# Performance work log

Measured on AMD Instinct MI355X. Metric: run time of the kernel, lower is better.

## Reference

```python
import jax, jax.numpy as jnp
import numpy as np

B, LQ, LK, QD, KD, VD, H = 8, 128, 1024, 128, 128, 128, 128
NEG_INF = -1e6  # d2l masked_softmax fill value


def setup_inputs() -> dict:
    key = jax.random.key(0)
    k1, k2, k3, k4, k5, k6, k7 = jax.random.split(key, 7)
    return {
        "queries": jax.random.normal(k1, (B, LQ, QD), dtype=jnp.float32),
        "keys": jax.random.normal(k2, (B, LK, KD), dtype=jnp.float32),
        "values": jax.random.normal(k3, (B, LK, VD), dtype=jnp.float32),
        "valid_lens": jax.random.randint(k4, (B,), 0, LK),
        # learned params: torch Linear(in,out,bias=False); stored here as [in,out]
        "W_q": jax.random.normal(k5, (QD, H), dtype=jnp.float32) / np.sqrt(QD),
        "W_k": jax.random.normal(k6, (KD, H), dtype=jnp.float32) / np.sqrt(KD),
        "w_v": jax.random.normal(k7, (H,), dtype=jnp.float32) / np.sqrt(H),
    }


def reference(queries, keys, values, valid_lens, W_q, W_k, w_v):
    q = jnp.einsum("blq,qh->blh", queries, W_q)            # [B,Lq,H]
    k = jnp.einsum("bsk,kh->bsh", keys, W_k)               # [B,Lk,H]
    features = jnp.tanh(q[:, :, None, :] + k[:, None, :, :])  # [B,Lq,Lk,H]
    scores = jnp.einsum("blsh,h->bls", features, w_v)      # [B,Lq,Lk]
    mask = jnp.arange(LK)[None, None, :] < valid_lens[:, None, None]
    scores = jnp.where(mask, scores, NEG_INF)
    attn = jax.nn.softmax(scores, axis=-1)                 # dropout p=0.0 -> identity
    return jnp.einsum("bls,bsv->blv", attn, values)        # [B,Lq,Vd]
```

## Files before the change

### kernel.cpp

```cpp
#include <hip/hip_runtime.h>
#include <hip/hip_fp16.h>

#define B_   8
#define LQ_  128
#define LK_  1024
#define H_   128

__device__ float        g_eq  [B_ * LQ_ * H_];
__device__ uint4        g_ekT4[B_ * (H_ / 4) * (LK_ / 2)];
__device__ unsigned int g_vh  [B_ * LK_ * (H_ / 2)];

#define C2LOG2E 2.8853900817779268f

__global__ __launch_bounds__(256) void proj_conv(const float* __restrict__ q,
                                                 const float* __restrict__ k,
                                                 const float* __restrict__ Wq,
                                                 const float* __restrict__ Wk,
                                                 const float* __restrict__ values) {
    const int bx = blockIdx.x, ch = blockIdx.y;
    const int t = threadIdx.x;
    if (bx >= 288) {
        const int idx = ((bx - 288) + (ch << 9)) * 256 + t;
        float4 v = *(const float4*)(values + (size_t)idx * 4);
        __half2 p0 = __floats2half2_rn(v.x, v.y);
        __half2 p1 = __floats2half2_rn(v.z, v.w);
        *(uint2*)(g_vh + (size_t)idx * 2) =
            make_uint2(*(unsigned int*)&p0, *(unsigned int*)&p1);
        return;
    }
    __shared__ float Ws[H_ * 64];
    __shared__ float Xs[32 * H_];
    const bool isq = (bx < 32);
    const float* X; const float* W; int r0;
    if (isq) { X = q; W = Wq; r0 = bx * 32; }
    else     { X = k; W = Wk; r0 = (bx - 32) * 32; }

    #pragma unroll
    for (int u = 0; u < 8; ++u) {
        int p = u * 256 + t;
        int kk = p >> 4, c4 = p & 15;
        *(float4*)(Ws + kk * 64 + c4 * 4) = *(const float4*)(W + kk * H_ + ch * 64 + c4 * 4);
    }
    #pragma unroll
    for (int u = 0; u < 4; ++u) {
        int idx = u * 256 + t;
        int r = idx >> 5, c = idx & 31;
        *(float4*)(Xs + r * H_ + c * 4) = *(const float4*)(X + (size_t)(r0 + r) * H_ + c * 4);
    }
    __syncthreads();

    const int rr = t >> 4;
    const int cc = t & 15;
    float acc[2][4] = {};
    #pragma unroll 4
    for (int kk = 0; kk < H_; ++kk) {
        float4 w4 = *(const float4*)(Ws + kk * 64 + cc * 4);
        float x0 = Xs[(rr * 2) * H_ + kk];
        float x1 = Xs[(rr * 2 + 1) * H_ + kk];
        acc[0][0] = fmaf(x0, w4.x, acc[0][0]); acc[0][1] = fmaf(x0, w4.y, acc[0][1]);
        acc[0][2] = fmaf(x0, w4.z, acc[0][2]); acc[0][3] = fmaf(x0, w4.w, acc[0][3]);
        acc[1][0] = fmaf(x1, w4.x, acc[1][0]); acc[1][1] = fmaf(x1, w4.y, acc[1][1]);
        acc[1][2] = fmaf(x1, w4.z, acc[1][2]); acc[1][3] = fmaf(x1, w4.w, acc[1][3]);
    }
    if (isq) {
        #pragma unroll
        for (int i = 0; i < 2; ++i) {
            float4 o;
            o.x = __builtin_amdgcn_exp2f(acc[i][0] * C2LOG2E);
            o.y = __builtin_amdgcn_exp2f(acc[i][1] * C2LOG2E);
            o.z = __builtin_amdgcn_exp2f(acc[i][2] * C2LOG2E);
            o.w = __builtin_amdgcn_exp2f(acc[i][3] * C2LOG2E);
            *(float4*)(g_eq + (size_t)(r0 + rr * 2 + i) * H_ + ch * 64 + cc * 4) = o;
        }
    } else {
        const int b  = r0 >> 10;
        const int s0 = (r0 & 1023) + rr * 2;
        const int h4 = ch * 16 + cc;
        uint4 pk;
        #pragma unroll
        for (int j = 0; j < 4; ++j) {
            float e0 = __builtin_amdgcn_exp2f(acc[0][j] * C2LOG2E);
            float e1 = __builtin_amdgcn_exp2f(acc[1][j] * C2LOG2E);
            __half2 p = __floats2half2_rn(e0, e1);
            ((unsigned int*)&pk)[j] = *(unsigned int*)&p;
        }
        g_ekT4[((size_t)b * (H_ / 4) + h4) * (LK_ / 2) + (s0 >> 1)] = pk;
    }
}

__global__ __launch_bounds__(512, 8) void fused_attn(const int* __restrict__ valid_lens,
                                                     const float* __restrict__ w_v,
                                                     float* __restrict__ out) {
    __shared__ float sc[LK_];
    __shared__ float sred[8];
    __shared__ float rinv_s;
    __shared__ float part[16][H_];
    const int t = threadIdx.x;
    const int lane = t & 63, wid = t >> 6;
    const int b = blockIdx.x >> 7, l = blockIdx.x & 127;
    int valid = valid_lens[b];
    valid = min(max(valid, 0), LK_);

    const int s0 = 2 * t;
    float e0 = 0.0f, e1 = 0.0f;
    if (valid == 0) {
        for (int i = t; i < LK_; i += 512) sc[i] = 1.0f;
    } else if (s0 < valid) {
        const float* __restrict__ q0 = g_eq + (size_t)(b * LQ_ + l) * H_;
        const uint4* __restrict__ ek = g_ekT4 + (size_t)b * (H_ / 4) * (LK_ / 2) + t;
        float a0 = 0.0f, a1 = 0.0f;
        #pragma unroll
        for (int hb = 0; hb < 4; ++hb) {
            uint4 r[8];
            #pragma unroll
            for (int i = 0; i < 8; ++i)
                r[i] = ek[(size_t)(hb * 8 + i) * (LK_ / 2)];
            #pragma unroll
            for (int i = 0; i < 8; ++i) {
                #pragma unroll
                for (int j = 0; j < 4; ++j) {
                    unsigned int uj = ((const unsigned int*)&r[i])[j];
                    float2 ef = __half22float2(*(const __half2*)&uj);
                    const int h = (hb * 8 + i) * 4 + j;
                    const float qh = q0[h], wh = w_v[h];
                    a0 = fmaf(wh, __builtin_amdgcn_rcpf(fmaf(qh, ef.x, 1.0f)), a0);
                    a1 = fmaf(wh, __builtin_amdgcn_rcpf(fmaf(qh, ef.y, 1.0f)), a1);
                }
            }
        }
        e0 = __builtin_amdgcn_exp2f(a0 * (-2.0f * 1.44269504f));
        float e1f = __builtin_amdgcn_exp2f(a1 * (-2.0f * 1.44269504f));
        *(float2*)(sc + s0) = make_float2(e0, e1f);
        e1 = (s0 + 1 < valid) ? e1f : 0.0f;
    }
    float ps = e0 + e1;
    #pragma unroll
    for (int kk = 32; kk; kk >>= 1) ps += __shfl_xor(ps, kk, 64);
    if (lane == 0) sred[wid] = ps;
    __syncthreads();
    if (t == 0) {
        float s8 = ((sred[0] + sred[1]) + (sred[2] + sred[3]))
                 + ((sred[4] + sred[5]) + (sred[6] + sred[7]));
        rinv_s = (valid == 0) ? (1.0f / 1024.0f) : (1.0f / s8);
    }
    __syncthreads();
    const float rinv = rinv_s;
    const int n = (valid == 0) ? LK_ : valid;

    const int c = t >> 5;
    const int v4 = t & 31;
    const uint2* vb = (const uint2*)g_vh + (size_t)b * LK_ * (H_ / 4) + v4;
    float ax = 0.0f, ay = 0.0f, az = 0.0f, aw = 0.0f;
    int s = c;
    for (; s + 16 * 7 < n; s += 16 * 8) {
        uint2 r[8];
        #pragma unroll
        for (int i = 0; i < 8; ++i)
            r[i] = vb[(size_t)(s + 16 * i) * (H_ / 4)];
        #pragma unroll
        for (int i = 0; i < 8; ++i) {
            float2 v01 = __half22float2(*(const __half2*)&r[i].x);
            float2 v23 = __half22float2(*(const __half2*)&r[i].y);
            float w = sc[s + 16 * i];
            ax = fmaf(w, v01.x, ax); ay = fmaf(w, v01.y, ay);
            az = fmaf(w, v23.x, az); aw = fmaf(w, v23.y, aw);
        }
    }
    for (; s < n; s += 16) {
        uint2 u = vb[(size_t)s * (H_ / 4)];
        float2 v01 = __half22float2(*(const __half2*)&u.x);
        float2 v23 = __half22float2(*(const __half2*)&u.y);
        float w = sc[s];
        ax = fmaf(w, v01.x, ax); ay = fmaf(w, v01.y, ay);
        az = fmaf(w, v23.x, az); aw = fmaf(w, v23.y, aw);
    }
    *(float4*)(&part[c][4 * v4]) = make_float4(ax, ay, az, aw);
    __syncthreads();
    if (t < H_) {
        float o = 0.0f;
        #pragma unroll
        for (int cc2 = 0; cc2 < 16; ++cc2) o += part[cc2][t];
        out[(b * LQ_ + l) * H_ + t] = o * rinv;
    }
}

extern "C" void kernel_launch(void* const* d_in, const int* in_sizes, int n_in,
                              void* d_out, int out_size, void* d_ws, size_t ws_size,
                              hipStream_t stream) {
    const float* queries    = (const float*)d_in[0];
    const float* keys       = (const float*)d_in[1];
    const float* values     = (const float*)d_in[2];
    const int*   valid_lens = (const int*)d_in[3];
    const float* W_q        = (const float*)d_in[4];
    const float* W_k        = (const float*)d_in[5];
    const float* w_v        = (const float*)d_in[6];
    float* out = (float*)d_out;
    (void)d_ws; (void)ws_size; (void)in_sizes; (void)n_in; (void)out_size;

    proj_conv <<<dim3(800, 2), 256, 0, stream>>>(queries, keys, W_q, W_k, values);
    fused_attn<<<1024, 512, 0, stream>>>(valid_lens, w_v, out);
}
```

Before: 33.93 us.

## Process two query rows per block to reuse key and value loads

Each fused_attn block now handles two adjacent query rows, so the transposed fp16 key tile and the fp16 value rows are loaded once and used for both rows. The grid is halved to 512 blocks, and shared memory and accumulators are doubled. The score phase is dominated by rcp (transcendental) ops, which do not shrink, so the main saving is halved global/L2 traffic for keys and values. The cost is more registers and LDS per block (occupancy hint lowered from 8 to 4) and fewer blocks to spread across CUs.

```diff
diff --git a/kernel.cpp b/kernel.cpp
--- a/kernel.cpp
+++ b/kernel.cpp
@@ -88,27 +88,28 @@
     }
 }
 
-__global__ __launch_bounds__(512, 8) void fused_attn(const int* __restrict__ valid_lens,
+__global__ __launch_bounds__(512, 4) void fused_attn(const int* __restrict__ valid_lens,
                                                      const float* __restrict__ w_v,
                                                      float* __restrict__ out) {
-    __shared__ float sc[LK_];
-    __shared__ float sred[8];
-    __shared__ float rinv_s;
-    __shared__ float part[16][H_];
+    __shared__ float scA[LK_], scB[LK_];
+    __shared__ float sredA[8], sredB[8];
+    __shared__ float rinvs[2];
+    __shared__ float part[16][2][H_];
     const int t = threadIdx.x;
     const int lane = t & 63, wid = t >> 6;
-    const int b = blockIdx.x >> 7, l = blockIdx.x & 127;
+    const int b = blockIdx.x >> 6, l0 = (blockIdx.x & 63) * 2;
     int valid = valid_lens[b];
     valid = min(max(valid, 0), LK_);
 
     const int s0 = 2 * t;
-    float e0 = 0.0f, e1 = 0.0f;
+    float p0 = 0.0f, p1 = 0.0f;
     if (valid == 0) {
-        for (int i = t; i < LK_; i += 512) sc[i] = 1.0f;
+        for (int i = t; i < LK_; i += 512) { scA[i] = 1.0f; scB[i] = 1.0f; }
     } else if (s0 < valid) {
-        const float* __restrict__ q0 = g_eq + (size_t)(b * LQ_ + l) * H_;
+        const float* __restrict__ q0 = g_eq + (size_t)(b * LQ_ + l0) * H_;
+        const float* __restrict__ q1 = q0 + H_;
         const uint4* __restrict__ ek = g_ekT4 + (size_t)b * (H_ / 4) * (LK_ / 2) + t;
-        float a0 = 0.0f, a1 = 0.0f;
+        float a00 = 0.0f, a01 = 0.0f, a10 = 0.0f, a11 = 0.0f;
         #pragma unroll
         for (int hb = 0; hb < 4; ++hb) {
             uint4 r[8];
@@ -122,35 +123,46 @@
                     unsigned int uj = ((const unsigned int*)&r[i])[j];
                     float2 ef = __half22float2(*(const __half2*)&uj);
                     const int h = (hb * 8 + i) * 4 + j;
-                    const float qh = q0[h], wh = w_v[h];
-                    a0 = fmaf(wh, __builtin_amdgcn_rcpf(fmaf(qh, ef.x, 1.0f)), a0);
-                    a1 = fmaf(wh, __builtin_amdgcn_rcpf(fmaf(qh, ef.y, 1.0f)), a1);
+                    const float qa = q0[h], qb = q1[h], wh = w_v[h];
+                    a00 = fmaf(wh, __builtin_amdgcn_rcpf(fmaf(qa, ef.x, 1.0f)), a00);
+                    a01 = fmaf(wh, __builtin_amdgcn_rcpf(fmaf(qa, ef.y, 1.0f)), a01);
+                    a10 = fmaf(wh, __builtin_amdgcn_rcpf(fmaf(qb, ef.x, 1.0f)), a10);
+                    a11 = fmaf(wh, __builtin_amdgcn_rcpf(fmaf(qb, ef.y, 1.0f)), a11);
                 }
             }
         }
-        e0 = __builtin_amdgcn_exp2f(a0 * (-2.0f * 1.44269504f));
-        float e1f = __builtin_amdgcn_exp2f(a1 * (-2.0f * 1.44269504f));
-        *(float2*)(sc + s0) = make_float2(e0, e1f);
-        e1 = (s0 + 1 < valid) ? e1f : 0.0f;
-    }
-    float ps = e0 + e1;
+        const float c = -2.0f * 1.44269504f;
+        float e00 = __builtin_amdgcn_exp2f(a00 * c);
+        float e01 = __builtin_amdgcn_exp2f(a01 * c);
+        float e10 = __builtin_amdgcn_exp2f(a10 * c);
+        float e11 = __builtin_amdgcn_exp2f(a11 * c);
+        *(float2*)(scA + s0) = make_float2(e00, e01);
+        *(float2*)(scB + s0) = make_float2(e10, e11);
+        const bool odd_ok = (s0 + 1 < valid);
+        p0 = e00 + (odd_ok ? e01 : 0.0f);
+        p1 = e10 + (odd_ok ? e11 : 0.0f);
+    }
     #pragma unroll
-    for (int kk = 32; kk; kk >>= 1) ps += __shfl_xor(ps, kk, 64);
-    if (lane == 0) sred[wid] = ps;
-    __syncthreads();
-    if (t == 0) {
-        float s8 = ((sred[0] + sred[1]) + (sred[2] + sred[3]))
-                 + ((sred[4] + sred[5]) + (sred[6] + sred[7]));
-        rinv_s = (valid == 0) ? (1.0f / 1024.0f) : (1.0f / s8);
-    }
-    __syncthreads();
-    const float rinv = rinv_s;
+    for (int kk = 32; kk; kk >>= 1) {
+        p0 += __shfl_xor(p0, kk, 64);
+        p1 += __shfl_xor(p1, kk, 64);
+    }
+    if (lane == 0) { sredA[wid] = p0; sredB[wid] = p1; }
+    __syncthreads();
+    if (t < 2) {
+        const float* sr = t ? sredB : sredA;
+        float s8 = ((sr[0] + sr[1]) + (sr[2] + sr[3]))
+                 + ((sr[4] + sr[5]) + (sr[6] + sr[7]));
+        rinvs[t] = (valid == 0) ? (1.0f / 1024.0f) : (1.0f / s8);
+    }
+    __syncthreads();
     const int n = (valid == 0) ? LK_ : valid;
 
     const int c = t >> 5;
     const int v4 = t & 31;
     const uint2* vb = (const uint2*)g_vh + (size_t)b * LK_ * (H_ / 4) + v4;
-    float ax = 0.0f, ay = 0.0f, az = 0.0f, aw = 0.0f;
+    float ax0 = 0.0f, ay0 = 0.0f, az0 = 0.0f, aw0 = 0.0f;
+    float ax1 = 0.0f, ay1 = 0.0f, az1 = 0.0f, aw1 = 0.0f;
     int s = c;
     for (; s + 16 * 7 < n; s += 16 * 8) {
         uint2 r[8];
@@ -161,26 +173,32 @@
         for (int i = 0; i < 8; ++i) {
             float2 v01 = __half22float2(*(const __half2*)&r[i].x);
             float2 v23 = __half22float2(*(const __half2*)&r[i].y);
-            float w = sc[s + 16 * i];
-            ax = fmaf(w, v01.x, ax); ay = fmaf(w, v01.y, ay);
-            az = fmaf(w, v23.x, az); aw = fmaf(w, v23.y, aw);
+            float w0 = scA[s + 16 * i], w1 = scB[s + 16 * i];
+            ax0 = fmaf(w0, v01.x, ax0); ay0 = fmaf(w0, v01.y, ay0);
+            az0 = fmaf(w0, v23.x, az0); aw0 = fmaf(w0, v23.y, aw0);
+            ax1 = fmaf(w1, v01.x, ax1); ay1 = fmaf(w1, v01.y, ay1);
+            az1 = fmaf(w1, v23.x, az1); aw1 = fmaf(w1, v23.y, aw1);
         }
     }
     for (; s < n; s += 16) {
         uint2 u = vb[(size_t)s * (H_ / 4)];
         float2 v01 = __half22float2(*(const __half2*)&u.x);
         float2 v23 = __half22float2(*(const __half2*)&u.y);
-        float w = sc[s];
-        ax = fmaf(w, v01.x, ax); ay = fmaf(w, v01.y, ay);
-        az = fmaf(w, v23.x, az); aw = fmaf(w, v23.y, aw);
-    }
-    *(float4*)(&part[c][4 * v4]) = make_float4(ax, ay, az, aw);
-    __syncthreads();
-    if (t < H_) {
+        float w0 = scA[s], w1 = scB[s];
+        ax0 = fmaf(w0, v01.x, ax0); ay0 = fmaf(w0, v01.y, ay0);
+        az0 = fmaf(w0, v23.x, az0); aw0 = fmaf(w0, v23.y, aw0);
+        ax1 = fmaf(w1, v01.x, ax1); ay1 = fmaf(w1, v01.y, ay1);
+        az1 = fmaf(w1, v23.x, az1); aw1 = fmaf(w1, v23.y, aw1);
+    }
+    *(float4*)(&part[c][0][4 * v4]) = make_float4(ax0, ay0, az0, aw0);
+    *(float4*)(&part[c][1][4 * v4]) = make_float4(ax1, ay1, az1, aw1);
+    __syncthreads();
+    if (t < 256) {
+        const int rr = t >> 7, v = t & 127;
         float o = 0.0f;
         #pragma unroll
-        for (int cc2 = 0; cc2 < 16; ++cc2) o += part[cc2][t];
-        out[(b * LQ_ + l) * H_ + t] = o * rinv;
+        for (int cc2 = 0; cc2 < 16; ++cc2) o += part[cc2][rr][v];
+        out[(b * LQ_ + l0 + rr) * H_ + v] = o * rinvs[rr];
     }
 }
 
@@ -198,5 +216,5 @@
     (void)d_ws; (void)ws_size; (void)in_sizes; (void)n_in; (void)out_size;
 
     proj_conv <<<dim3(800, 2), 256, 0, stream>>>(queries, keys, W_q, W_k, values);
-    fused_attn<<<1024, 512, 0, stream>>>(valid_lens, w_v, out);
+    fused_attn<<<512, 512, 0, stream>>>(valid_lens, w_v, out);
 }
```

After: 34.31 us. Within noise of the previous version (+1.1%).
